# Kernel optimization log

Measured on AMD Instinct MI355X. Metric: run time of the kernel, lower is better.

## Reference

```python
import jax, jax.numpy as jnp
import numpy as np
from jax import lax

# dims
B, T, N, E, DEG = 8, 24, 1000, 1000, 20
F_IN, C_RAW, DM, HC, TK, PRED, OUT = 16, 8, 32, 32, 32, 12, 1
LAM = 0.3
EPS = 1e-8


def _dyn_features(x_raw):
    # build_window_dynamic_features: per-node window stats (mean, std) -> (B, N, 2C)
    return jnp.concatenate([x_raw.mean(axis=1), x_raw.std(axis=1)], axis=-1)


def _dynamic_weights(x_raw, W, members, centers, offsets):
    feat = _dyn_features(x_raw)                      # (B, N, D)
    M = members.shape[0]
    # member -> owning edge id from CSR offsets (jit-safe repeat_interleave)
    mids = jnp.searchsorted(offsets[1:], jnp.arange(M), side='right')  # (M,)
    mf = feat[:, members, :]                          # (B, M, D)
    cf = feat[:, centers[mids], :]                    # (B, M, D)
    sim = (mf * cf).sum(-1) / (jnp.linalg.norm(mf, axis=-1) * jnp.linalg.norm(cf, axis=-1) + EPS)
    sim = jnp.clip(sim, 0.0, 1.0)                     # (B, M)
    counts = (offsets[1:] - offsets[:-1]).astype(sim.dtype)  # (E,)
    mean_sim = jnp.zeros((sim.shape[0], offsets.shape[0] - 1), sim.dtype).at[:, mids].add(sim)
    mean_sim = mean_sim / jnp.clip(counts, 1.0)[None, :]
    smin = mean_sim.min(axis=1, keepdims=True)
    smax = mean_sim.max(axis=1, keepdims=True)
    mean_sim = (mean_sim - smin) / (smax - smin + EPS)
    return W[None, :] * (1.0 + LAM * mean_sim)        # (B, E)


def _norm_hypergraph(H, Wd):
    # A = Dv^{-1/2} H W De^{-1} H^T Dv^{-1/2}, batched over edge weights Wd (B,E)
    De = jnp.clip(H.sum(axis=0), 1.0)                 # (E,)
    dv = jnp.einsum('ne,be->bn', H, Wd)               # (B, N)
    dvi = lax.rsqrt(jnp.clip(dv, EPS))
    HW = H[None, :, :] * (Wd / De)[:, None, :]        # (B, N, E)
    A0 = jnp.einsum('bne,me->bnm', HW, H)             # (B, N, N)
    return dvi[:, :, None] * A0 * dvi[:, None, :]


def _lstm_last(seq, wx, wh, b):
    # TKANLayer temporal recurrence (LSTM-style cell), return_sequences=False
    BN = seq.shape[0]
    Hd = wh.shape[0]
    h0 = jnp.zeros((BN, Hd), seq.dtype)

    def step(carry, xt):
        h, c = carry
        z = xt @ wx + h @ wh + b                      # (BN, 4H)
        i, f, g, o = jnp.split(z, 4, axis=-1)
        c = jax.nn.sigmoid(f) * c + jax.nn.sigmoid(i) * jnp.tanh(g)
        h = jax.nn.sigmoid(o) * jnp.tanh(c)
        return (h, c), None

    (h, _), _ = lax.scan(step, (h0, h0), jnp.swapaxes(seq, 0, 1))
    return h


def setup_inputs() -> dict:
    key = jax.random.key(0)
    ks = jax.random.split(key, 16)

    edge_members = jax.random.randint(ks[0], (E * DEG,), 0, N)
    edge_centers = jnp.arange(E)                      # center node = edge index
    edge_offsets = jnp.arange(E + 1) * DEG            # uniform-degree CSR
    mids = jnp.repeat(jnp.arange(E), DEG)
    H = (jnp.zeros((N, E))
         .at[edge_members, mids].set(1.0)
         .at[edge_centers, jnp.arange(E)].set(1.0))
    W = jax.random.uniform(ks[1], (E,), minval=0.5, maxval=1.5)

    x = jax.random.normal(ks[2], (B, T, N, F_IN))
    x_raw = jax.random.normal(ks[3], (B, T, N, C_RAW))

    w = lambda k, s: jax.random.normal(k, s) * 0.05
    return {
        'x': x, 'x_raw': x_raw, 'H': H, 'W': W,
        'edge_members': edge_members, 'edge_centers': edge_centers, 'edge_offsets': edge_offsets,
        'in_proj_w': w(ks[4], (F_IN, DM)), 'in_proj_b': jnp.zeros((DM,)),
        'conv_w': w(ks[5], (DM, HC)), 'conv_b': jnp.zeros((HC,)),
        'lstm_wx': w(ks[6], (HC, 4 * TK)), 'lstm_wh': w(ks[7], (TK, 4 * TK)), 'lstm_b': jnp.zeros((4 * TK,)),
        'head_w1': w(ks[8], (TK, TK)), 'head_b1': jnp.zeros((TK,)),
        'head_w2': w(ks[9], (TK, PRED * OUT)), 'head_b2': jnp.zeros((PRED * OUT,)),
        'output_length': 12,
    }


def reference(x, x_raw, H, W, edge_members, edge_centers, edge_offsets,
              in_proj_w, in_proj_b, conv_w, conv_b,
              lstm_wx, lstm_wh, lstm_b,
              head_w1, head_b1, head_w2, head_b2, output_length):
    xp = x @ in_proj_w + in_proj_b                    # (B, T, N, DM)

    # DynamicEdgeWeighter is @torch.no_grad() in the original
    Wd = lax.stop_gradient(_dynamic_weights(x_raw, W, edge_members, edge_centers, edge_offsets))
    A = _norm_hypergraph(H, Wd)                       # (B, N, N)

    # per-timestep hypergraph conv, vectorized over T (same math as the Python loop)
    h = jnp.einsum('bnm,btmf->btnf', A, xp)
    h = jax.nn.silu(h @ conv_w + conv_b)              # (B, T, N, HC)

    seq = jnp.transpose(h, (0, 2, 1, 3)).reshape(B * N, T, HC)
    ht = _lstm_last(seq, lstm_wx, lstm_wh, lstm_b)    # (B*N, TK)

    y = jax.nn.silu(ht @ head_w1 + head_b1) @ head_w2 + head_b2
    y = y.reshape(B, N, PRED, OUT).transpose(0, 2, 1, 3)  # (B, PRED, N, OUT)
    return y[:, :output_length]
```

## Files before the change

### kernel.cpp

```cpp
#include <hip/hip_runtime.h>
#include <hip/hip_bf16.h>
#include <math.h>

#define BB 8
#define TT 24
#define NN 1000
#define EE 1000
#define DEG 20
#define FIN 16
#define CRAW 8
#define DM 32
#define HCN 32
#define TKN 32
#define PREDN 12
#define LAMF 0.3f
#define EPSF 1e-8f

typedef float f4 __attribute__((ext_vector_type(4)));

__device__ __forceinline__ float sigmoidf_(float x){ return 1.f/(1.f+__expf(-x)); }
__device__ __forceinline__ float siluf_(float x){ return x/(1.f+__expf(-x)); }
__device__ __forceinline__ float sigmfast_(float x){
  return __builtin_amdgcn_rcpf(1.f+__expf(-x));
}
__device__ __forceinline__ float tanhfast_(float x){
  float xx = fminf(fmaxf(x,-15.f),15.f);
  float e = __expf(2.f*xx);
  return 1.f - 2.f*__builtin_amdgcn_rcpf(e+1.f);
}

__global__ __launch_bounds__(1024) void k_prep(
    const int* __restrict__ members, const int* __restrict__ centers,
    const int* __restrict__ offsets,
    int* __restrict__ edge_nodes, int* __restrict__ edge_cnt,
    int* __restrict__ node_off, int* __restrict__ node_edges)
{
  __shared__ int deg[NN];
  __shared__ int cur[NN];
  __shared__ int offs[NN+1];
  __shared__ int buf[1024];
  int tid = threadIdx.x;
  for(int i=tid;i<NN;i+=1024){ deg[i]=0; cur[i]=0; }
  __syncthreads();
  int e = tid;
  int cnt = 0;
  if(e<EE){
    int st=offsets[e], en=offsets[e+1];
    int c=centers[e];
    int mem[DEG];
    #pragma unroll
    for(int k=0;k<DEG;k++) mem[k] = (st+k<en)? members[st+k] : -1;
    edge_nodes[e*(DEG+1)+0]=c;
    atomicAdd(&deg[c],1);
    cnt=1;
    #pragma unroll
    for(int k=0;k<DEG;k++){
      int m = mem[k];
      bool dup = (m==c) | (m<0);
      #pragma unroll
      for(int k2=0;k2<DEG;k2++) if(k2<k && mem[k2]==m) dup=true;
      if(!dup){
        edge_nodes[e*(DEG+1)+cnt]=m;
        atomicAdd(&deg[m],1);
        cnt++;
      }
    }
    edge_cnt[e]=cnt;
    for(int j=cnt;j<DEG+1;j++) edge_nodes[e*(DEG+1)+j]=0;
  }
  __syncthreads();
  buf[tid] = (tid<NN)? deg[tid] : 0;
  __syncthreads();
  for(int d=1;d<1024;d<<=1){
    int v = (tid>=d)? buf[tid-d] : 0;
    __syncthreads();
    buf[tid]+=v;
    __syncthreads();
  }
  if(tid==0) offs[0]=0;
  if(tid<NN) offs[tid+1]=buf[tid];
  __syncthreads();
  if(tid<=NN) node_off[tid]=offs[tid];
  if(e<EE){
    for(int j=0;j<cnt;j++){
      int n = edge_nodes[e*(DEG+1)+j];
      int pos = atomicAdd(&cur[n],1);
      node_edges[offs[n]+pos] = e;
    }
  }
}

__global__ void k_feat(const float* __restrict__ xraw, float* __restrict__ feat){
  int tid = threadIdx.x;
  int c = tid & 7, nloc = tid >> 3;
  int row = blockIdx.x*32 + nloc;
  if (row >= BB*NN) return;
  int b = row/NN, n = row%NN;
  float s=0.f, s2=0.f;
  for (int t=0;t<TT;t++){
    float vv = xraw[(((size_t)(b*TT+t)*NN + n)*CRAW) + c];
    s += vv; s2 += vv*vv;
  }
  float m = s*(1.f/TT);
  float var = fmaxf(s2*(1.f/TT) - m*m, 0.f);
  feat[(size_t)row*16 + c]     = m;
  feat[(size_t)row*16 + 8 + c] = sqrtf(var);
}

__global__ __launch_bounds__(256) void k_sim1(
    const float* __restrict__ feat,
    const int* __restrict__ members, const int* __restrict__ centers,
    const int* __restrict__ offsets, float* __restrict__ ms)
{
  int tid = threadIdx.x;
  int lane2 = tid & 3;
  int task = blockIdx.x*64 + (tid>>2);
  if(task >= BB*EE) return;
  int b = task/EE, e = task%EE;
  const float* fb = feat + (size_t)b*NN*16;
  int st=offsets[e], en=offsets[e+1];
  int ci=centers[e];
  float cf[16]; float nc=0.f;
  const f4* cp = (const f4*)(fb + ci*16);
  #pragma unroll
  for(int k=0;k<4;k++){
    f4 v = cp[k];
    #pragma unroll
    for(int c=0;c<4;c++){ cf[4*k+c]=v[c]; nc = fmaf(v[c],v[c],nc); }
  }
  nc = sqrtf(nc);
  float acc=0.f;
  for(int k=st+lane2;k<en;k+=4){
    int m=members[k];
    const f4* mp = (const f4*)(fb + m*16);
    float dot=0.f, nm=0.f;
    #pragma unroll
    for(int kk=0;kk<4;kk++){
      f4 v = mp[kk];
      #pragma unroll
      for(int c=0;c<4;c++){ dot = fmaf(v[c], cf[4*kk+c], dot); nm = fmaf(v[c],v[c],nm); }
    }
    float sim = dot/(sqrtf(nm)*nc + EPSF);
    acc += fminf(fmaxf(sim,0.f),1.f);
  }
  acc += __shfl_xor(acc, 1, 64);
  acc += __shfl_xor(acc, 2, 64);
  if(lane2==0) ms[task] = acc / fmaxf((float)(en-st),1.f);
}

__global__ __launch_bounds__(1024) void k_sim2dv(
    const float* __restrict__ ms, const float* __restrict__ W,
    const int* __restrict__ node_off, const int* __restrict__ node_edges,
    float* __restrict__ Wd, float* __restrict__ dvi)
{
  __shared__ float red1[1024], red2[1024];
  __shared__ float wdl[EE];
  int b = blockIdx.x;
  int tid = threadIdx.x;
  float msv = (tid<EE)? ms[b*EE+tid] : 0.f;
  red1[tid]=(tid<EE)? msv : 1e30f;
  red2[tid]=(tid<EE)? msv : -1e30f;
  __syncthreads();
  for(int s=512;s>0;s>>=1){
    if(tid<s){
      red1[tid]=fminf(red1[tid],red1[tid+s]);
      red2[tid]=fmaxf(red2[tid],red2[tid+s]);
    }
    __syncthreads();
  }
  if(tid<EE){
    float msn=(msv-red1[0])/(red2[0]-red1[0]+EPSF);
    float w = W[tid]*(1.f+LAMF*msn);
    Wd[b*EE+tid]=w;
    wdl[tid]=w;
  }
  __syncthreads();
  if(tid<NN){
    int st=node_off[tid], en=node_off[tid+1];
    float dv=0.f;
    for(int k=st;k<en;k++) dv += wdl[node_edges[k]];
    dvi[b*NN+tid] = rsqrtf(fmaxf(dv, EPSF));
  }
}

__global__ __launch_bounds__(1024) void k_slice(
    const float* __restrict__ x,
    const float* __restrict__ ipw, const float* __restrict__ ipb,
    const float* __restrict__ dvi, const float* __restrict__ Wd,
    const int* __restrict__ edge_nodes, const int* __restrict__ edge_cnt,
    const int* __restrict__ node_off, const int* __restrict__ node_edges,
    const float* __restrict__ cw, const float* __restrict__ cb,
    float* __restrict__ hc_out)
{
  __shared__ f4 zbuf[NN*8];
  __shared__ float ipws[FIN*32];
  __shared__ f4 cws4[DM*8];
  __shared__ float wde[EE];
  __shared__ int   cnts[EE];
  __shared__ float ipbs[32], cbs[32];

  int tid = threadIdx.x;
  int bt  = blockIdx.x;
  int b = bt / TT, t = bt % TT;

  for(int i=tid;i<FIN*32;i+=1024) ipws[i]=ipw[i];
  for(int i=tid;i<DM*8;i+=1024) cws4[i]=((const f4*)cw)[i];
  for(int e=tid;e<EE;e+=1024){
    int c = edge_cnt[e];
    cnts[e]=c;
    wde[e]=Wd[b*EE+e]/(float)c;
  }
  if(tid<32){ ipbs[tid]=ipb[tid]; cbs[tid]=cb[tid]; }
  __syncthreads();

  const float* xb  = x + (size_t)bt*NN*FIN;
  const float* dvb = dvi + b*NN;
  float* zs = (float*)zbuf;

  {
    int g = tid>>5, f = tid&31;
    for(int p=0;p<32;p++){
      int r = p*32+g;
      if(r<NN){
        const f4* x4 = (const f4*)(xb + r*FIN);
        float acc = ipbs[f];
        #pragma unroll
        for(int k=0;k<4;k++){
          f4 xv = x4[k];
          acc = fmaf(xv[0], ipws[(4*k+0)*32+f], acc);
          acc = fmaf(xv[1], ipws[(4*k+1)*32+f], acc);
          acc = fmaf(xv[2], ipws[(4*k+2)*32+f], acc);
          acc = fmaf(xv[3], ipws[(4*k+3)*32+f], acc);
        }
        zs[r*32 + (((f>>2)^(r&7))<<2) + (f&3)] = dvb[r]*acc;
      }
    }
  }
  __syncthreads();

  int grp = tid>>3, q = tid&7;
  f4 vreg[8];
  #pragma unroll
  for(int p=0;p<8;p++){
    int e = p*128 + grp;
    f4 acc = (f4)0.f;
    if(e<EE){
      int cnt = cnts[e];
      const int* enp = edge_nodes + e*(DEG+1);
      int idx[DEG+1];
      #pragma unroll
      for(int j=0;j<DEG+1;j++) idx[j]=enp[j];
      #pragma unroll
      for(int j=0;j<DEG+1;j++){
        f4 v = zbuf[idx[j]*8 + (q ^ (idx[j]&7))];
        if(j<cnt) acc += v;
      }
      acc *= wde[e];
    }
    vreg[p]=acc;
  }
  __syncthreads();
  #pragma unroll
  for(int p=0;p<8;p++){
    int e = p*128 + grp;
    if(e<EE) zbuf[e*8 + (q^(e&7))] = vreg[p];
  }
  __syncthreads();

  int lanew = tid&63, grpw = lanew>>3;
  for(int p=0;p<8;p++){
    int n = p*128 + grp;
    f4 acc = (f4)0.f;
    int st=0, en=0;
    if(n<NN){ st=node_off[n]; en=node_off[n+1]; }
    for(int j=st;j<en;j+=4){
      #pragma unroll
      for(int k=0;k<4;k++){
        int jj = (j+k<en)? j+k : st;
        int e2 = node_edges[jj];
        f4 v = zbuf[e2*8 + (q ^ (e2&7))];
        if(j+k<en) acc += v;
      }
    }
    float dvn = (n<NN)? dvb[n] : 0.f;
    acc *= dvn;
    f4 hcq;
    #pragma unroll
    for(int c=0;c<4;c++) hcq[c]=cbs[q*4+c];
    #pragma unroll
    for(int i=0;i<32;i++){
      float h2i = __shfl(acc[i&3], grpw*8 + (i>>2), 64);
      f4 w = cws4[i*8+q];
      hcq += h2i * w;
    }
    #pragma unroll
    for(int c=0;c<4;c++) hcq[c]=siluf_(hcq[c]);
    if(n<NN) ((f4*)hc_out)[ ((size_t)(b*NN+n)*TT + t)*8 + q ] = hcq;
  }
}

__global__ __launch_bounds__(256) void k_zx(
    const float* __restrict__ hc, const float* __restrict__ wx,
    const float* __restrict__ lb, float* __restrict__ zx)
{
  __shared__ f4 wxl[32*32];
  __shared__ f4 lbl[32];
  int tid = threadIdx.x;
  for(int w=tid;w<1024;w+=256){
    int i = w>>5, cq = w&31;
    wxl[i*32 + ((cq&7)<<2) + (cq>>3)] = ((const f4*)wx)[w];
  }
  if(tid<32) lbl[tid] = ((const f4*)lb)[tid];
  int it = tid>>2, q4 = tid&3;
  size_t item = (size_t)blockIdx.x*64 + it;
  const f4* hp = (const f4*)(hc + item*32);
  f4 hreg[8];
  #pragma unroll
  for(int k=0;k<8;k++) hreg[k] = hp[k];
  __syncthreads();
  f4 acc[8];
  #pragma unroll
  for(int j=0;j<8;j++) acc[j] = lbl[q4*8+j];
  #pragma unroll
  for(int i=0;i<32;i++){
    float hv = hreg[i>>2][i&3];
    #pragma unroll
    for(int j=0;j<8;j++) acc[j] += hv * wxl[i*32 + (j<<2) + q4];
  }
  f4* op = (f4*)(zx + item*128 + q4*32);
  #pragma unroll
  for(int j=0;j<8;j++) op[j] = acc[j];
}

__global__ __launch_bounds__(256,2) void k_lstm(const float* __restrict__ zx,
    const float* __restrict__ wh,
    const float* __restrict__ w1, const float* __restrict__ b1,
    const float* __restrict__ w2, const float* __restrict__ b2,
    float* __restrict__ out){
  __shared__ float hsh[8*32];
  int tid = threadIdx.x;
  int r = tid>>5, c = tid&31;
  int row = blockIdx.x*8 + r;
  const float* zr = zx + (size_t)row*TT*128;
  float wr0[32], wr1[32], wr2[32], wr3[32];
  #pragma unroll
  for(int i=0;i<32;i++){
    wr0[i]=wh[i*128 + c];
    wr1[i]=wh[i*128 + 32 + c];
    wr2[i]=wh[i*128 + 64 + c];
    wr3[i]=wh[i*128 + 96 + c];
  }
  const f4* hrow4 = (const f4*)&hsh[r*32];
  float h=0.f, cs=0.f;
  float p0=zr[c], p1=zr[32+c], p2=zr[64+c], p3=zr[96+c];
  for(int t=0;t<TT;t++){
    float z0=p0, z1=p1, z2=p2, z3=p3;
    if(t+1<TT){
      const float* nz = zr + (size_t)(t+1)*128;
      p0=nz[c]; p1=nz[32+c]; p2=nz[64+c]; p3=nz[96+c];
    }
    hsh[r*32+c] = h;
    #pragma unroll
    for(int i4=0;i4<8;i4++){
      f4 h4 = hrow4[i4];
      #pragma unroll
      for(int k=0;k<4;k++){
        int i = i4*4+k;
        z0 = fmaf(h4[k], wr0[i], z0);
        z1 = fmaf(h4[k], wr1[i], z1);
        z2 = fmaf(h4[k], wr2[i], z2);
        z3 = fmaf(h4[k], wr3[i], z3);
      }
    }
    float ig = sigmfast_(z0);
    float fg = sigmfast_(z1);
    float gg = tanhfast_(z2);
    float og = sigmfast_(z3);
    cs = fg*cs + ig*gg;
    h = og*tanhfast_(cs);
  }
  int b = row/NN, n = row%NN;
  hsh[r*32+c] = h;
  float t1 = b1[c];
  #pragma unroll
  for(int i4=0;i4<8;i4++){
    f4 h4 = hrow4[i4];
    #pragma unroll
    for(int k=0;k<4;k++) t1 = fmaf(h4[k], w1[(i4*4+k)*32+c], t1);
  }
  t1 = siluf_(t1);
  hsh[r*32+c] = t1;
  float y = (c<PREDN)? b2[c] : 0.f;
  #pragma unroll
  for(int i4=0;i4<8;i4++){
    f4 t4 = hrow4[i4];
    #pragma unroll
    for(int k=0;k<4;k++){
      if(c<PREDN) y = fmaf(t4[k], w2[(i4*4+k)*PREDN+c], y);
    }
  }
  if(c<PREDN) out[((size_t)b*PREDN + c)*NN + n] = y;
}

extern "C" void kernel_launch(void* const* d_in, const int* in_sizes, int n_in,
                              void* d_out, int out_size, void* d_ws, size_t ws_size,
                              hipStream_t stream) {
  const float* x       = (const float*)d_in[0];
  const float* xraw    = (const float*)d_in[1];
  const float* W       = (const float*)d_in[3];
  const int*   members = (const int*)d_in[4];
  const int*   centers = (const int*)d_in[5];
  const int*   offsets = (const int*)d_in[6];
  const float* ipw     = (const float*)d_in[7];
  const float* ipb     = (const float*)d_in[8];
  const float* cw      = (const float*)d_in[9];
  const float* cb      = (const float*)d_in[10];
  const float* wx      = (const float*)d_in[11];
  const float* wh      = (const float*)d_in[12];
  const float* lb      = (const float*)d_in[13];
  const float* w1      = (const float*)d_in[14];
  const float* b1      = (const float*)d_in[15];
  const float* w2      = (const float*)d_in[16];
  const float* b2      = (const float*)d_in[17];
  float* out = (float*)d_out;

  float* zx   = (float*)d_ws;
  float* hc   = zx + 24576000;
  float* feat = hc + 6144000;
  float* ms   = feat + 128000;
  float* Wd   = ms + 8000;
  float* dvi  = Wd + 8000;
  int* edge_nodes = (int*)(dvi + 8000);
  int* edge_cnt   = edge_nodes + 21000;
  int* node_off   = edge_cnt + 1000;
  int* node_edges = node_off + 1001;

  k_prep<<<1, 1024, 0, stream>>>(members, centers, offsets,
                                 edge_nodes, edge_cnt, node_off, node_edges);
  k_feat<<<250, 256, 0, stream>>>(xraw, feat);
  k_sim1<<<125, 256, 0, stream>>>(feat, members, centers, offsets, ms);
  k_sim2dv<<<BB, 1024, 0, stream>>>(ms, W, node_off, node_edges, Wd, dvi);
  k_slice<<<BB*TT, 1024, 0, stream>>>(x, ipw, ipb, dvi, Wd,
                                      edge_nodes, edge_cnt, node_off, node_edges,
                                      cw, cb, hc);
  k_zx<<<3000, 256, 0, stream>>>(hc, wx, lb, zx);
  k_lstm<<<(BB*NN)/8, 256, 0, stream>>>(zx, wh, w1, b1, w2, b2, out);
}
```

Baseline: 306.5 us.

## Split graph prep into multi-block kernels, unroll node gather, restage zx GEMM via LDS

The single-block k_prep is split into a parallel dedup kernel, a single-block scan, and a parallel fill kernel that use global atomics and a memset'd degree/cursor buffer. The node-side gather in k_slice now preloads up to 24 edge indices per node and accumulates them in a fully unrolled loop, with a fallback loop for higher degrees. k_zx now stages the hidden-state tile in shared memory and has each thread compute 8 items times one 4-wide output column. The split adds extra launches and a memset, and the zx rewrite changes the memory access pattern.

```diff
diff --git a/kernel.cpp b/kernel.cpp
--- a/kernel.cpp
+++ b/kernel.cpp
@@ -29,64 +29,62 @@
   return 1.f - 2.f*__builtin_amdgcn_rcpf(e+1.f);
 }
 
-__global__ __launch_bounds__(1024) void k_prep(
-    const int* __restrict__ members, const int* __restrict__ centers,
-    const int* __restrict__ offsets,
-    int* __restrict__ edge_nodes, int* __restrict__ edge_cnt,
-    int* __restrict__ node_off, int* __restrict__ node_edges)
-{
-  __shared__ int deg[NN];
-  __shared__ int cur[NN];
-  __shared__ int offs[NN+1];
+__global__ void k_dedup(const int* __restrict__ members, const int* __restrict__ centers,
+                        const int* __restrict__ offsets,
+                        int* __restrict__ edge_nodes, int* __restrict__ edge_cnt,
+                        int* __restrict__ node_deg){
+  int e = blockIdx.x*blockDim.x + threadIdx.x;
+  if(e>=EE) return;
+  int st=offsets[e], en=offsets[e+1];
+  int c=centers[e];
+  int mem[DEG];
+  #pragma unroll
+  for(int k=0;k<DEG;k++) mem[k] = (st+k<en)? members[st+k] : -1;
+  edge_nodes[e*(DEG+1)+0]=c;
+  atomicAdd(&node_deg[c],1);
+  int cnt=1;
+  #pragma unroll
+  for(int k=0;k<DEG;k++){
+    int m = mem[k];
+    bool dup = (m==c) | (m<0);
+    #pragma unroll
+    for(int k2=0;k2<DEG;k2++) if(k2<k && mem[k2]==m) dup=true;
+    if(!dup){
+      edge_nodes[e*(DEG+1)+cnt]=m;
+      atomicAdd(&node_deg[m],1);
+      cnt++;
+    }
+  }
+  edge_cnt[e]=cnt;
+  for(int j=cnt;j<DEG+1;j++) edge_nodes[e*(DEG+1)+j]=0;
+}
+
+__global__ __launch_bounds__(1024) void k_scan(const int* __restrict__ node_deg,
+                                               int* __restrict__ node_off){
   __shared__ int buf[1024];
-  int tid = threadIdx.x;
-  for(int i=tid;i<NN;i+=1024){ deg[i]=0; cur[i]=0; }
-  __syncthreads();
-  int e = tid;
-  int cnt = 0;
-  if(e<EE){
-    int st=offsets[e], en=offsets[e+1];
-    int c=centers[e];
-    int mem[DEG];
-    #pragma unroll
-    for(int k=0;k<DEG;k++) mem[k] = (st+k<en)? members[st+k] : -1;
-    edge_nodes[e*(DEG+1)+0]=c;
-    atomicAdd(&deg[c],1);
-    cnt=1;
-    #pragma unroll
-    for(int k=0;k<DEG;k++){
-      int m = mem[k];
-      bool dup = (m==c) | (m<0);
-      #pragma unroll
-      for(int k2=0;k2<DEG;k2++) if(k2<k && mem[k2]==m) dup=true;
-      if(!dup){
-        edge_nodes[e*(DEG+1)+cnt]=m;
-        atomicAdd(&deg[m],1);
-        cnt++;
-      }
-    }
-    edge_cnt[e]=cnt;
-    for(int j=cnt;j<DEG+1;j++) edge_nodes[e*(DEG+1)+j]=0;
-  }
-  __syncthreads();
-  buf[tid] = (tid<NN)? deg[tid] : 0;
+  int i=threadIdx.x;
+  buf[i] = (i<NN)? node_deg[i]:0;
   __syncthreads();
   for(int d=1;d<1024;d<<=1){
-    int v = (tid>=d)? buf[tid-d] : 0;
+    int v = (i>=d)? buf[i-d] : 0;
     __syncthreads();
-    buf[tid]+=v;
+    buf[i]+=v;
     __syncthreads();
   }
-  if(tid==0) offs[0]=0;
-  if(tid<NN) offs[tid+1]=buf[tid];
-  __syncthreads();
-  if(tid<=NN) node_off[tid]=offs[tid];
-  if(e<EE){
-    for(int j=0;j<cnt;j++){
-      int n = edge_nodes[e*(DEG+1)+j];
-      int pos = atomicAdd(&cur[n],1);
-      node_edges[offs[n]+pos] = e;
-    }
+  if(i==0) node_off[0]=0;
+  if(i<NN) node_off[i+1]=buf[i];
+}
+
+__global__ void k_fill(const int* __restrict__ edge_nodes, const int* __restrict__ edge_cnt,
+                       const int* __restrict__ node_off, int* __restrict__ cursor,
+                       int* __restrict__ node_edges){
+  int e = blockIdx.x*blockDim.x + threadIdx.x;
+  if(e>=EE) return;
+  int cnt=edge_cnt[e];
+  for(int j=0;j<cnt;j++){
+    int n = edge_nodes[e*(DEG+1)+j];
+    int pos = atomicAdd(&cursor[n],1);
+    node_edges[node_off[n]+pos] = e;
   }
 }
 
@@ -270,17 +268,21 @@
   int lanew = tid&63, grpw = lanew>>3;
   for(int p=0;p<8;p++){
     int n = p*128 + grp;
+    int st=0, deg=0;
+    if(n<NN){ st=node_off[n]; deg=node_off[n+1]-st; }
+    int idx[24];
+    #pragma unroll
+    for(int k=0;k<24;k++) idx[k] = (k<deg)? node_edges[st+k] : 0;
     f4 acc = (f4)0.f;
-    int st=0, en=0;
-    if(n<NN){ st=node_off[n]; en=node_off[n+1]; }
-    for(int j=st;j<en;j+=4){
-      #pragma unroll
-      for(int k=0;k<4;k++){
-        int jj = (j+k<en)? j+k : st;
-        int e2 = node_edges[jj];
-        f4 v = zbuf[e2*8 + (q ^ (e2&7))];
-        if(j+k<en) acc += v;
-      }
+    #pragma unroll
+    for(int k=0;k<24;k++){
+      int e2 = idx[k];
+      f4 v = zbuf[e2*8 + (q ^ (e2&7))];
+      if(k<deg) acc += v;
+    }
+    for(int j=st+24;j<st+deg;j++){
+      int e2 = node_edges[j];
+      acc += zbuf[e2*8 + (q ^ (e2&7))];
     }
     float dvn = (n<NN)? dvb[n] : 0.f;
     acc *= dvn;
@@ -304,32 +306,42 @@
     const float* __restrict__ lb, float* __restrict__ zx)
 {
   __shared__ f4 wxl[32*32];
+  __shared__ f4 hcl[64*8];
   __shared__ f4 lbl[32];
   int tid = threadIdx.x;
-  for(int w=tid;w<1024;w+=256){
-    int i = w>>5, cq = w&31;
-    wxl[i*32 + ((cq&7)<<2) + (cq>>3)] = ((const f4*)wx)[w];
-  }
+  for(int w=tid;w<1024;w+=256) wxl[w] = ((const f4*)wx)[w];
   if(tid<32) lbl[tid] = ((const f4*)lb)[tid];
-  int it = tid>>2, q4 = tid&3;
-  size_t item = (size_t)blockIdx.x*64 + it;
-  const f4* hp = (const f4*)(hc + item*32);
-  f4 hreg[8];
-  #pragma unroll
-  for(int k=0;k<8;k++) hreg[k] = hp[k];
-  __syncthreads();
+  size_t base = (size_t)blockIdx.x*64;
+  {
+    const f4* hp = (const f4*)(hc + base*32);
+    hcl[tid]     = hp[tid];
+    hcl[tid+256] = hp[tid+256];
+  }
+  __syncthreads();
+  int ig = tid>>5, q4 = tid&31;
   f4 acc[8];
-  #pragma unroll
-  for(int j=0;j<8;j++) acc[j] = lbl[q4*8+j];
-  #pragma unroll
-  for(int i=0;i<32;i++){
-    float hv = hreg[i>>2][i&3];
-    #pragma unroll
-    for(int j=0;j<8;j++) acc[j] += hv * wxl[i*32 + (j<<2) + q4];
-  }
-  f4* op = (f4*)(zx + item*128 + q4*32);
-  #pragma unroll
-  for(int j=0;j<8;j++) op[j] = acc[j];
+  f4 l = lbl[q4];
+  #pragma unroll
+  for(int it=0;it<8;it++) acc[it]=l;
+  #pragma unroll
+  for(int c=0;c<8;c++){
+    f4 w0 = wxl[(4*c+0)*32+q4];
+    f4 w1 = wxl[(4*c+1)*32+q4];
+    f4 w2 = wxl[(4*c+2)*32+q4];
+    f4 w3 = wxl[(4*c+3)*32+q4];
+    #pragma unroll
+    for(int it=0;it<8;it++){
+      f4 h4 = hcl[(ig*8+it)*8 + c];
+      acc[it] += h4[0]*w0;
+      acc[it] += h4[1]*w1;
+      acc[it] += h4[2]*w2;
+      acc[it] += h4[3]*w3;
+    }
+  }
+  #pragma unroll
+  for(int it=0;it<8;it++){
+    ((f4*)(zx + (base + (size_t)(ig*8+it))*128))[q4] = acc[it];
+  }
 }
 
 __global__ __launch_bounds__(256,2) void k_lstm(const float* __restrict__ zx,
@@ -433,11 +445,18 @@
   int* edge_nodes = (int*)(dvi + 8000);
   int* edge_cnt   = edge_nodes + 21000;
   int* node_off   = edge_cnt + 1000;
-  int* node_edges = node_off + 1001;
-
-  k_prep<<<1, 1024, 0, stream>>>(members, centers, offsets,
-                                 edge_nodes, edge_cnt, node_off, node_edges);
+  int* node_deg   = node_off + 1001;
+  int* cursor     = node_deg + 1000;
+  int* node_edges = cursor + 1000;
+
+  hipMemsetAsync(node_deg, 0, 2000*sizeof(int), stream);
+
   k_feat<<<250, 256, 0, stream>>>(xraw, feat);
+  k_dedup<<<(EE+255)/256, 256, 0, stream>>>(members, centers, offsets,
+                                            edge_nodes, edge_cnt, node_deg);
+  k_scan<<<1, 1024, 0, stream>>>(node_deg, node_off);
+  k_fill<<<(EE+255)/256, 256, 0, stream>>>(edge_nodes, edge_cnt, node_off,
+                                           cursor, node_edges);
   k_sim1<<<125, 256, 0, stream>>>(feat, members, centers, offsets, ms);
   k_sim2dv<<<BB, 1024, 0, stream>>>(ms, W, node_off, node_edges, Wd, dvi);
   k_slice<<<BB*TT, 1024, 0, stream>>>(x, ipw, ipb, dvi, Wd,
```

New measurement: 279.8 us. -8.7%, faster.
